# Kernel optimization log

Hardware: AMD Instinct MI355X
Metric: run time of the kernel (lower is better)

The kernel has to match this reference:

```python
import jax, jax.numpy as jnp
import numpy as np

K = 8  # w_size

def setup_inputs() -> dict:
    key = jax.random.key(0)
    mat = jax.random.normal(key, (1, 64, 1024, 1024), dtype=jnp.float32)
    return {"mat": mat}

def reference(mat) -> jnp.ndarray:
    # Intended math of SADecompLayer: for each channel, for each KxK block w:
    #   s = w + flip_lr(w) + flip_ud(w) + flip_lr(flip_ud(w))
    #   out_block = (s + rot90(s)) / 8   (dihedral-group symmetrization)
    x = mat[0]  # [C, H, W]
    C, H, W = x.shape
    hb, wb = H // K, W // K
    # [C, hb, wb, K, K] blocks
    b = x.reshape(C, hb, K, wb, K).transpose(0, 1, 3, 2, 4)
    s = b + b[..., ::-1] + b[..., ::-1, :] + b[..., ::-1, ::-1]
    r = jnp.rot90(s, k=1, axes=(-2, -1))  # CCW rotation of each block
    out = (s + r) * jnp.float32(0.125)
    # back to [C, H, W]
    return out.transpose(0, 1, 3, 2, 4).reshape(C, H, W)
```

## Files before the change

kernel.cpp:

```cpp
#include <hip/hip_runtime.h>


constexpr int KW = 8;
constexpr int W  = 1024;
constexpr int W4 = W / 4;
constexpr int WB = W / KW;

typedef float v4f __attribute__((ext_vector_type(4)));

__global__ __launch_bounds__(256) void sadecomp_kernel(
    const float* __restrict__ in, float* __restrict__ out, int nhalf) {
    int t = blockIdx.x * blockDim.x + threadIdx.x;
    if (t >= nhalf) return;

    const int half = t & 1;
    const int blk  = t >> 1;
    const int bx   = blk & (WB - 1);
    const int rest = blk >> 7;
    const int base = rest * (KW * W4) + bx * 2 + half;

    const v4f* __restrict__ inp  = reinterpret_cast<const v4f*>(in);
    v4f* __restrict__       outp = reinterpret_cast<v4f*>(out);

    v4f f[8];
#pragma unroll
    for (int r = 0; r < 8; ++r) f[r] = inp[base + r * W4];

    v4f wv[4];
#pragma unroll
    for (int a = 0; a < 4; ++a) wv[a] = f[a] + f[7 - a];

    float u[4][4];
#pragma unroll
    for (int a = 0; a < 4; ++a) {
        float px = __shfl_xor(wv[a].x, 1);
        float py = __shfl_xor(wv[a].y, 1);
        float pz = __shfl_xor(wv[a].z, 1);
        float pw = __shfl_xor(wv[a].w, 1);
        u[a][0] = wv[a].x + pw;
        u[a][1] = wv[a].y + pz;
        u[a][2] = wv[a].z + py;
        u[a][3] = wv[a].w + px;
    }

    const bool rightHalf = (half != 0);
    float T[4][4];
#pragma unroll
    for (int a = 0; a < 4; ++a) {
#pragma unroll
        for (int b = 0; b < 4; ++b) {
            float second = rightHalf ? u[3 - b][3 - a] : u[b][a];
            T[a][b] = (u[a][b] + second) * 0.125f;
        }
    }

#pragma unroll
    for (int i = 0; i < 4; ++i) {
        v4f o;
        o.x = T[i][0]; o.y = T[i][1]; o.z = T[i][2]; o.w = T[i][3];
        __builtin_nontemporal_store(o, &outp[base + i * W4]);
        __builtin_nontemporal_store(o, &outp[base + (7 - i) * W4]);
    }
}

extern "C" void kernel_launch(void* const* d_in, const int* in_sizes, int n_in,
                              void* d_out, int out_size, void* d_ws, size_t ws_size,
                              hipStream_t stream) {
    const float* in = (const float*)d_in[0];
    float* out = (float*)d_out;

    const int nhalf = (out_size / (KW * KW)) * 2;
    const int block = 256;
    const int grid = (nhalf + block - 1) / block;
    sadecomp_kernel<<<grid, block, 0, stream>>>(in, out, nhalf);
}
```

Baseline: 81.92 us.

## Process four half-blocks per thread with register double-buffered prefetch

Each thread now handles four half-blocks in a grid-stride loop and loads the next half-block's eight rows into registers before computing and storing the current one. The grid is cut by a factor of four. The goal is more memory loads in flight per thread and less launch and scheduling overhead. In exchange it uses more registers, which can lower occupancy. It also drops the bounds check, so it assumes the problem size divides evenly.

Result: no change. 81.57 us (median of 2 runs) (-0.4%).

```diff
diff --git a/kernel.cpp b/kernel.cpp
--- a/kernel.cpp
+++ b/kernel.cpp
@@ -5,61 +5,80 @@
 constexpr int W  = 1024;
 constexpr int W4 = W / 4;
 constexpr int WB = W / KW;
+constexpr int ITERS = 4;
 
 typedef float v4f __attribute__((ext_vector_type(4)));
 
+__device__ __forceinline__ int half_block_base(int t) {
+    int half = t & 1;
+    int blk  = t >> 1;
+    int bx   = blk & (WB - 1);
+    int rest = blk >> 7;
+    return rest * (KW * W4) + bx * 2 + half;
+}
+
 __global__ __launch_bounds__(256) void sadecomp_kernel(
-    const float* __restrict__ in, float* __restrict__ out, int nhalf) {
-    int t = blockIdx.x * blockDim.x + threadIdx.x;
-    if (t >= nhalf) return;
-
-    const int half = t & 1;
-    const int blk  = t >> 1;
-    const int bx   = blk & (WB - 1);
-    const int rest = blk >> 7;
-    const int base = rest * (KW * W4) + bx * 2 + half;
+    const float* __restrict__ in, float* __restrict__ out) {
+    const int t0     = blockIdx.x * blockDim.x + threadIdx.x;
+    const int stride = gridDim.x * blockDim.x;
+    const bool rightHalf = (t0 & 1) != 0;
 
     const v4f* __restrict__ inp  = reinterpret_cast<const v4f*>(in);
     v4f* __restrict__       outp = reinterpret_cast<v4f*>(out);
 
-    v4f f[8];
+    v4f cur[8];
+    int base = half_block_base(t0);
 #pragma unroll
-    for (int r = 0; r < 8; ++r) f[r] = inp[base + r * W4];
-
-    v4f wv[4];
-#pragma unroll
-    for (int a = 0; a < 4; ++a) wv[a] = f[a] + f[7 - a];
-
-    float u[4][4];
-#pragma unroll
-    for (int a = 0; a < 4; ++a) {
-        float px = __shfl_xor(wv[a].x, 1);
-        float py = __shfl_xor(wv[a].y, 1);
-        float pz = __shfl_xor(wv[a].z, 1);
-        float pw = __shfl_xor(wv[a].w, 1);
-        u[a][0] = wv[a].x + pw;
-        u[a][1] = wv[a].y + pz;
-        u[a][2] = wv[a].z + py;
-        u[a][3] = wv[a].w + px;
-    }
-
-    const bool rightHalf = (half != 0);
-    float T[4][4];
-#pragma unroll
-    for (int a = 0; a < 4; ++a) {
-#pragma unroll
-        for (int b = 0; b < 4; ++b) {
-            float second = rightHalf ? u[3 - b][3 - a] : u[b][a];
-            T[a][b] = (u[a][b] + second) * 0.125f;
-        }
-    }
+    for (int r = 0; r < 8; ++r) cur[r] = inp[base + r * W4];
 
 #pragma unroll
-    for (int i = 0; i < 4; ++i) {
-        v4f o;
-        o.x = T[i][0]; o.y = T[i][1]; o.z = T[i][2]; o.w = T[i][3];
-        __builtin_nontemporal_store(o, &outp[base + i * W4]);
-        __builtin_nontemporal_store(o, &outp[base + (7 - i) * W4]);
+    for (int k = 0; k < ITERS; ++k) {
+        v4f nxt[8];
+        int nbase = 0;
+        if (k + 1 < ITERS) {
+            nbase = half_block_base(t0 + (k + 1) * stride);
+#pragma unroll
+            for (int r = 0; r < 8; ++r) nxt[r] = inp[nbase + r * W4];
+        }
+
+        v4f wv[4];
+#pragma unroll
+        for (int a = 0; a < 4; ++a) wv[a] = cur[a] + cur[7 - a];
+
+        float u[4][4];
+#pragma unroll
+        for (int a = 0; a < 4; ++a) {
+            float px = __shfl_xor(wv[a].x, 1);
+            float py = __shfl_xor(wv[a].y, 1);
+            float pz = __shfl_xor(wv[a].z, 1);
+            float pw = __shfl_xor(wv[a].w, 1);
+            u[a][0] = wv[a].x + pw;
+            u[a][1] = wv[a].y + pz;
+            u[a][2] = wv[a].z + py;
+            u[a][3] = wv[a].w + px;
+        }
+
+        float T[4][4];
+#pragma unroll
+        for (int a = 0; a < 4; ++a) {
+#pragma unroll
+            for (int b = 0; b < 4; ++b) {
+                float second = rightHalf ? u[3 - b][3 - a] : u[b][a];
+                T[a][b] = (u[a][b] + second) * 0.125f;
+            }
+        }
+
+#pragma unroll
+        for (int i = 0; i < 4; ++i) {
+            v4f o;
+            o.x = T[i][0]; o.y = T[i][1]; o.z = T[i][2]; o.w = T[i][3];
+            __builtin_nontemporal_store(o, &outp[base + i * W4]);
+            __builtin_nontemporal_store(o, &outp[base + (7 - i) * W4]);
+        }
+
+        base = nbase;
+#pragma unroll
+        for (int r = 0; r < 8; ++r) cur[r] = nxt[r];
     }
 }
 
@@ -71,6 +90,6 @@
 
     const int nhalf = (out_size / (KW * KW)) * 2;
     const int block = 256;
-    const int grid = (nhalf + block - 1) / block;
-    sadecomp_kernel<<<grid, block, 0, stream>>>(in, out, nhalf);
+    const int grid = nhalf / (block * ITERS);
+    sadecomp_kernel<<<grid, block, 0, stream>>>(in, out);
 }
```
